# Kernel optimization log

Hardware: AMD Instinct MI355X
Metric: run time of the kernel (lower is better)

## Reference

```python
import jax, jax.numpy as jnp
import numpy as np

N_NODES = 100000
N_EDGES = 600000
VOCAB = 5000
NUM_GRAPHS = 2000
NUM_CLASSES = 10


def setup_inputs() -> dict:
    key = jax.random.key(0)
    ks = jax.random.split(key, 12)
    x = jax.random.randint(ks[0], (N_NODES,), 0, VOCAB, dtype=jnp.int32)
    edge_index = jax.random.randint(ks[1], (2, N_EDGES), 0, N_NODES, dtype=jnp.int32)
    batch = jnp.sort(jax.random.randint(ks[2], (N_NODES,), 0, NUM_GRAPHS, dtype=jnp.int32))
    emb = jax.random.normal(ks[3], (VOCAB, 64), dtype=jnp.float32) * 0.1
    W1 = jax.random.normal(ks[4], (64, 128), dtype=jnp.float32) * (1.0 / np.sqrt(64))
    b1 = jnp.zeros((128,), dtype=jnp.float32)
    W2 = jax.random.normal(ks[5], (128, 128), dtype=jnp.float32) * (1.0 / np.sqrt(128))
    b2 = jnp.zeros((128,), dtype=jnp.float32)
    Wlin = jax.random.normal(ks[6], (128, NUM_CLASSES), dtype=jnp.float32) * (1.0 / np.sqrt(128))
    blin = jnp.zeros((NUM_CLASSES,), dtype=jnp.float32)
    return {"x": x, "edge_index": edge_index, "batch": batch, "num_graphs": NUM_GRAPHS,
            "emb": emb, "W1": W1, "b1": b1, "W2": W2, "b2": b2, "Wlin": Wlin, "blin": blin}


def reference(x, edge_index, batch, num_graphs, emb, W1, b1, W2, b2, Wlin, blin):
    N = x.shape[0]
    loops = jnp.arange(N, dtype=edge_index.dtype)
    src = jnp.concatenate([edge_index[0], loops])  # message sources (j)
    dst = jnp.concatenate([edge_index[1], loops])  # aggregation targets (i)
    # GCN symmetric normalization with self-loops (PyG gcn_norm, source_to_target)
    deg = jax.ops.segment_sum(jnp.ones_like(dst, dtype=jnp.float32), dst, num_segments=N)
    dinv = jnp.where(deg > 0, jax.lax.rsqrt(deg), 0.0)
    norm = dinv[src] * dinv[dst]  # [E+N]

    def gcn(h, W, b):
        h = h @ W  # linear transform first (GCNConv order)
        msg = h[src] * norm[:, None]  # gather + scale, [E+N, F]
        return jax.ops.segment_sum(msg, dst, num_segments=N) + b

    h = emb[x]  # [N, 64]
    h = jax.nn.relu(gcn(h, W1, b1))
    h = jax.nn.relu(gcn(h, W2, b2))
    g = jax.ops.segment_max(h, batch, num_segments=num_graphs)  # global_max_pool
    return g @ Wlin + blin
```

## Files before the change

### kernel.cpp

```cpp
#include <hip/hip_runtime.h>
#include <hip/hip_bf16.h>
#include <hip/hip_fp16.h>


typedef _Float16 h8 __attribute__((ext_vector_type(8)));
typedef float f32x4 __attribute__((ext_vector_type(4)));

__global__ __launch_bounds__(256) void k_zero(int4* __restrict__ deg, int n4i,
                                              int4* __restrict__ pool, int p4i) {
    int t = blockIdx.x * 256 + threadIdx.x;
    int4 z = make_int4(0, 0, 0, 0);
    if (t < n4i) deg[t] = z;
    if (t < p4i) pool[t] = z;
}

__global__ __launch_bounds__(256) void k_degprep(const int* __restrict__ dst, int* __restrict__ deg, int E,
                                                 const float* __restrict__ emb, __half2* __restrict__ e16,
                                                 const float* __restrict__ W1, _Float16* __restrict__ W1T,
                                                 const float* __restrict__ W2, _Float16* __restrict__ W2T,
                                                 int nEmbF, int gE, int nCast) {
    int bid = blockIdx.x;
    if (bid < gE) {
        int e = bid * 256 + threadIdx.x;
        if (e < E) atomicAdd(&deg[dst[e]], 1);
    } else if (bid < gE + nCast) {
        int t = (bid - gE) * 256 + threadIdx.x;
        if (t * 4 < nEmbF) {
            float4 v = *(const float4*)&emb[t * 4];
            e16[t * 2] = __floats2half2_rn(v.x, v.y);
            e16[t * 2 + 1] = __floats2half2_rn(v.z, v.w);
        }
    } else if (bid < gE + nCast + 32) {
        int t = (bid - gE - nCast) * 256 + threadIdx.x;
        int c = t >> 6, k = t & 63;
        W1T[c * 64 + k] = (_Float16)W1[k * 128 + c];
    } else {
        int t = (bid - gE - nCast - 32) * 256 + threadIdx.x;
        if (t < 128 * 128) {
            int c = t >> 7, k = t & 127;
            W2T[c * 128 + k] = (_Float16)W2[k * 128 + c];
        }
    }
}

__global__ __launch_bounds__(256) void k_scan1(const int* __restrict__ deg, int* __restrict__ exc,
                                               int* __restrict__ bsums, float* __restrict__ dinv, int N) {
    __shared__ int s[256];
    int i = blockIdx.x * 256 + threadIdx.x;
    int v = (i < N) ? deg[i] : 0;
    if (i < N) dinv[i] = rsqrtf((float)(v + 1));
    s[threadIdx.x] = v;
    __syncthreads();
    for (int off = 1; off < 256; off <<= 1) {
        int t = (threadIdx.x >= (unsigned)off) ? s[threadIdx.x - off] : 0;
        __syncthreads();
        s[threadIdx.x] += t;
        __syncthreads();
    }
    if (i < N) exc[i] = s[threadIdx.x] - v;
    if (threadIdx.x == 255) bsums[blockIdx.x] = s[255];
}

__global__ __launch_bounds__(512) void k_scan2(int* __restrict__ bsums, int nb) {
    __shared__ int s[512];
    int i = threadIdx.x;
    int v = (i < nb) ? bsums[i] : 0;
    s[i] = v;
    __syncthreads();
    for (int off = 1; off < 512; off <<= 1) {
        int t = (i >= off) ? s[i - off] : 0;
        __syncthreads();
        s[i] += t;
        __syncthreads();
    }
    if (i < nb) bsums[i] = s[i] - v;
}

__global__ __launch_bounds__(256) void k_scan3(int* __restrict__ rowstart, int* __restrict__ cursor,
                                               const int* __restrict__ bsums, int N, int E) {
    int i = blockIdx.x * 256 + threadIdx.x;
    if (i < N) {
        int r = rowstart[i] + bsums[blockIdx.x];
        rowstart[i] = r;
        cursor[i] = r;
    }
    if (i == 0 && blockIdx.x == 0) rowstart[N] = E;
}

__global__ __launch_bounds__(256) void k_fill(const int* __restrict__ src, const int* __restrict__ dst,
                                              const int* __restrict__ x, const float* __restrict__ dinv,
                                              int* __restrict__ cursor, int2* __restrict__ ed,
                                              int* __restrict__ cols, int E) {
    int e = blockIdx.x * 256 + threadIdx.x;
    if (e < E) {
        int d = dst[e];
        int s = src[e];
        int pos = atomicAdd(&cursor[d], 1);
        ed[pos] = make_int2(x[s], __float_as_int(dinv[s]));
        cols[pos] = s;
    }
}

__global__ __launch_bounds__(512) void k_mlp(const __half2* __restrict__ e16, const int* __restrict__ x,
                                             const float* __restrict__ dinv, const int* __restrict__ rs,
                                             const int2* __restrict__ ed, const _Float16* __restrict__ W1T,
                                             const float* __restrict__ b1, const _Float16* __restrict__ W2T,
                                             _Float16* __restrict__ P, int N) {
    __shared__ _Float16 Xs[32][72];
    __shared__ _Float16 Hs[32][136];
    int tid = threadIdx.x;
    int blk0 = blockIdx.x * 32;
    {
        int lane = tid & 31;
        int hw = tid >> 5;
        int p = lane >> 3;
        int f16 = lane & 7;
        const h8* e8 = (const h8*)e16;
        int nlA = hw * 2, nlB = nlA + 1;
        int gA = blk0 + nlA; if (gA >= N) gA = N - 1;
        int gB = blk0 + nlB; if (gB >= N) gB = N - 1;
        int cA0 = rs[gA], cA1 = rs[gA + 1];
        int cB0 = rs[gB], cB1 = rs[gB + 1];
        int baseA = (cA0 < cA1) ? cA1 - 1 : 0;
        int baseB = (cB0 < cB1) ? cB1 - 1 : 0;
        float dA = dinv[gA], dB = dinv[gB];
        h8 selfA = e8[(size_t)x[gA] * 8 + f16];
        h8 selfB = e8[(size_t)x[gB] * 8 + f16];
        float accA[8] = {}, accB[8] = {};
        {
            int eA0 = cA0 + p, eA1 = cA0 + 4 + p;
            int eB0 = cB0 + p, eB1 = cB0 + 4 + p;
            int2 rA0 = ed[(eA0 < cA1) ? eA0 : baseA];
            int2 rA1 = ed[(eA1 < cA1) ? eA1 : baseA];
            int2 rB0 = ed[(eB0 < cB1) ? eB0 : baseB];
            int2 rB1 = ed[(eB1 < cB1) ? eB1 : baseB];
            h8 tA0 = e8[(size_t)rA0.x * 8 + f16];
            h8 tA1 = e8[(size_t)rA1.x * 8 + f16];
            h8 tB0 = e8[(size_t)rB0.x * 8 + f16];
            h8 tB1 = e8[(size_t)rB1.x * 8 + f16];
            float wA0 = (eA0 < cA1) ? __int_as_float(rA0.y) : 0.f;
            float wA1 = (eA1 < cA1) ? __int_as_float(rA1.y) : 0.f;
            float wB0 = (eB0 < cB1) ? __int_as_float(rB0.y) : 0.f;
            float wB1 = (eB1 < cB1) ? __int_as_float(rB1.y) : 0.f;
#pragma unroll
            for (int f = 0; f < 8; ++f) {
                accA[f] = fmaf(wA1, (float)tA1[f], fmaf(wA0, (float)tA0[f], accA[f]));
                accB[f] = fmaf(wB1, (float)tB1[f], fmaf(wB0, (float)tB0[f], accB[f]));
            }
        }
        for (int eb = cA0 + 8; eb < cA1; eb += 8) {
            int e0 = eb + p, e1i = eb + 4 + p;
            int2 r0 = ed[(e0 < cA1) ? e0 : cA1 - 1];
            int2 r1 = ed[(e1i < cA1) ? e1i : cA1 - 1];
            h8 t0 = e8[(size_t)r0.x * 8 + f16];
            h8 t1 = e8[(size_t)r1.x * 8 + f16];
            float w0 = (e0 < cA1) ? __int_as_float(r0.y) : 0.f;
            float w1 = (e1i < cA1) ? __int_as_float(r1.y) : 0.f;
#pragma unroll
            for (int f = 0; f < 8; ++f)
                accA[f] = fmaf(w1, (float)t1[f], fmaf(w0, (float)t0[f], accA[f]));
        }
        for (int eb = cB0 + 8; eb < cB1; eb += 8) {
            int e0 = eb + p, e1i = eb + 4 + p;
            int2 r0 = ed[(e0 < cB1) ? e0 : cB1 - 1];
            int2 r1 = ed[(e1i < cB1) ? e1i : cB1 - 1];
            h8 t0 = e8[(size_t)r0.x * 8 + f16];
            h8 t1 = e8[(size_t)r1.x * 8 + f16];
            float w0 = (e0 < cB1) ? __int_as_float(r0.y) : 0.f;
            float w1 = (e1i < cB1) ? __int_as_float(r1.y) : 0.f;
#pragma unroll
            for (int f = 0; f < 8; ++f)
                accB[f] = fmaf(w1, (float)t1[f], fmaf(w0, (float)t0[f], accB[f]));
        }
        h8 yA, yB;
#pragma unroll
        for (int f = 0; f < 8; ++f) {
            float a = accA[f];
            a += __shfl_xor(a, 8);
            a += __shfl_xor(a, 16);
            float b = accB[f];
            b += __shfl_xor(b, 8);
            b += __shfl_xor(b, 16);
            yA[f] = (_Float16)(dA * fmaf(dA, (float)selfA[f], a));
            yB[f] = (_Float16)(dB * fmaf(dB, (float)selfB[f], b));
        }
        if (p == 0) {
            *(h8*)&Xs[nlA][f16 * 8] = yA;
            *(h8*)&Xs[nlB][f16 * 8] = yB;
        }
    }
    __syncthreads();
    int l = tid & 63, wid = tid >> 6;
    int r = l & 15, kg = l >> 4;
    int rb = wid & 1;
    int ch = wid >> 1;
    {
        f32x4 acc[2];
#pragma unroll
        for (int ct = 0; ct < 2; ++ct) acc[ct] = (f32x4){0.f, 0.f, 0.f, 0.f};
#pragma unroll
        for (int kc = 0; kc < 2; ++kc) {
            h8 a = *(const h8*)&Xs[rb * 16 + r][kc * 32 + kg * 8];
#pragma unroll
            for (int ct = 0; ct < 2; ++ct) {
                h8 b = *(const h8*)(W1T + (size_t)(ch * 32 + ct * 16 + r) * 64 + kc * 32 + kg * 8);
                acc[ct] = __builtin_amdgcn_mfma_f32_16x16x32_f16(a, b, acc[ct], 0, 0, 0);
            }
        }
#pragma unroll
        for (int ct = 0; ct < 2; ++ct) {
            float bias = b1[ch * 32 + ct * 16 + r];
#pragma unroll
            for (int i = 0; i < 4; ++i)
                Hs[rb * 16 + 4 * kg + i][ch * 32 + ct * 16 + r] =
                    (_Float16)fmaxf(acc[ct][i] + bias, 0.f);
        }
    }
    __syncthreads();
    {
        f32x4 acc[2];
#pragma unroll
        for (int ct = 0; ct < 2; ++ct) acc[ct] = (f32x4){0.f, 0.f, 0.f, 0.f};
#pragma unroll
        for (int kc = 0; kc < 4; ++kc) {
            h8 a = *(const h8*)&Hs[rb * 16 + r][kc * 32 + kg * 8];
#pragma unroll
            for (int ct = 0; ct < 2; ++ct) {
                h8 b = *(const h8*)(W2T + (size_t)(ch * 32 + ct * 16 + r) * 128 + kc * 32 + kg * 8);
                acc[ct] = __builtin_amdgcn_mfma_f32_16x16x32_f16(a, b, acc[ct], 0, 0, 0);
            }
        }
        float dv[4];
#pragma unroll
        for (int i = 0; i < 4; ++i) {
            int gr = blk0 + rb * 16 + 4 * kg + i;
            dv[i] = (gr < N) ? dinv[gr] : 0.f;
        }
#pragma unroll
        for (int ct = 0; ct < 2; ++ct) {
#pragma unroll
            for (int i = 0; i < 4; ++i) {
                int gr = blk0 + rb * 16 + 4 * kg + i;
                if (gr < N)
                    P[(size_t)gr * 128 + ch * 32 + ct * 16 + r] = (_Float16)(acc[ct][i] * dv[i]);
            }
        }
    }
}

__global__ __launch_bounds__(256) void k_agg2pool(const h8* __restrict__ P8, const int* __restrict__ batch,
                                                  const float* __restrict__ dinv, const int* __restrict__ rs,
                                                  const int* __restrict__ cols, const float* __restrict__ b2,
                                                  float* __restrict__ pool, int N, int G) {
    __shared__ int lpool[4][128];
    int tid = threadIdx.x;
    lpool[tid >> 7][tid & 127] = 0;
    lpool[(tid >> 7) + 2][tid & 127] = 0;
    __syncthreads();
    int lane = tid & 31;
    int p = lane >> 4;
    int s = lane & 15;
    int blk_n0 = blockIdx.x * 16;
    int gfirst = batch[(blk_n0 < N) ? blk_n0 : (N - 1)];
    int n0 = blk_n0 + (tid >> 5) * 2;
    if (n0 < N) {
        int nA = n0;
        int nB = (n0 + 1 < N) ? n0 + 1 : n0;
        int cA0 = rs[nA], cA1 = rs[nA + 1];
        int cB0 = rs[nB], cB1 = rs[nB + 1];
        bool hasA = cA0 < cA1, hasB = cB0 < cB1;
        h8 sA = P8[(size_t)nA * 16 + s];
        h8 sB = P8[(size_t)nB * 16 + s];
        float aA[8] = {}, aB[8] = {};
        {
            h8 tA[8], tB[8];
            float wA[8], wB[8];
#pragma unroll
            for (int i = 0; i < 8; ++i) {
                int ei = cA0 + 2 * i + p;
                int ec = (ei < cA1) ? ei : (hasA ? cA1 - 1 : 0);
                tA[i] = P8[(size_t)cols[ec] * 16 + s];
                wA[i] = (ei < cA1) ? 1.f : 0.f;
            }
#pragma unroll
            for (int i = 0; i < 8; ++i) {
                int ei = cB0 + 2 * i + p;
                int ec = (ei < cB1) ? ei : (hasB ? cB1 - 1 : 0);
                tB[i] = P8[(size_t)cols[ec] * 16 + s];
                wB[i] = (ei < cB1) ? 1.f : 0.f;
            }
#pragma unroll
            for (int i = 0; i < 8; ++i)
#pragma unroll
                for (int f = 0; f < 8; ++f) aA[f] = fmaf(wA[i], (float)tA[i][f], aA[f]);
#pragma unroll
            for (int i = 0; i < 8; ++i)
#pragma unroll
                for (int f = 0; f < 8; ++f) aB[f] = fmaf(wB[i], (float)tB[i][f], aB[f]);
        }
        for (int eb = cA0 + 16; eb < cA1; eb += 16) {
            h8 t[8];
            float w[8];
#pragma unroll
            for (int i = 0; i < 8; ++i) {
                int ei = eb + 2 * i + p;
                int ec = (ei < cA1) ? ei : cA1 - 1;
                t[i] = P8[(size_t)cols[ec] * 16 + s];
                w[i] = (ei < cA1) ? 1.f : 0.f;
            }
#pragma unroll
            for (int i = 0; i < 8; ++i)
#pragma unroll
                for (int f = 0; f < 8; ++f) aA[f] = fmaf(w[i], (float)t[i][f], aA[f]);
        }
        for (int eb = cB0 + 16; eb < cB1; eb += 16) {
            h8 t[8];
            float w[8];
#pragma unroll
            for (int i = 0; i < 8; ++i) {
                int ei = eb + 2 * i + p;
                int ec = (ei < cB1) ? ei : cB1 - 1;
                t[i] = P8[(size_t)cols[ec] * 16 + s];
                w[i] = (ei < cB1) ? 1.f : 0.f;
            }
#pragma unroll
            for (int i = 0; i < 8; ++i)
#pragma unroll
                for (int f = 0; f < 8; ++f) aB[f] = fmaf(w[i], (float)t[i][f], aB[f]);
        }
        float dA = dinv[nA], dB = dinv[nB];
        int gA = batch[nA], gB = batch[nB];
        float4 bb0 = *(const float4*)&b2[s * 8];
        float4 bb1 = *(const float4*)&b2[s * 8 + 4];
        float bv[8] = {bb0.x, bb0.y, bb0.z, bb0.w, bb1.x, bb1.y, bb1.z, bb1.w};
        float zA[8], zB[8];
#pragma unroll
        for (int f = 0; f < 8; ++f) {
            float a = aA[f] + __shfl_xor(aA[f], 16);
            float b = aB[f] + __shfl_xor(aB[f], 16);
            zA[f] = fmaxf(fmaf(dA, (float)sA[f] + a, bv[f]), 0.f);
            zB[f] = fmaxf(fmaf(dB, (float)sB[f] + b, bv[f]), 0.f);
        }
        auto emit = [&](int g, const float* m) {
            if (p != 0) return;
            int slot = g - gfirst;
            if (slot < 4) {
#pragma unroll
                for (int f = 0; f < 8; ++f) {
                    int ff = (f + s) & 7;
                    if (m[ff] > 0.f) atomicMax(&lpool[slot][s * 8 + ff], __float_as_int(m[ff]));
                }
            } else {
                float* pg = pool + (size_t)g * 128 + s * 8;
#pragma unroll
                for (int f = 0; f < 8; ++f)
                    if (m[f] > 0.f) atomicMax((int*)(pg + f), __float_as_int(m[f]));
            }
        };
        if (gA == gB) {
            float m[8];
#pragma unroll
            for (int f = 0; f < 8; ++f) m[f] = fmaxf(zA[f], zB[f]);
            emit(gA, m);
        } else {
            emit(gA, zA);
            emit(gB, zB);
        }
    }
    __syncthreads();
    {
        int f = tid & 127;
        for (int sl = tid >> 7; sl < 4; sl += 2) {
            int v = lpool[sl][f];
            if (v > 0) atomicMax((int*)&pool[(size_t)(gfirst + sl) * 128 + f], v);
        }
    }
}

__global__ __launch_bounds__(256) void k_final(const float* __restrict__ pool, const float* __restrict__ Wlin,
                                               const float* __restrict__ blin, float* __restrict__ out, int G) {
    int t = blockIdx.x * 256 + threadIdx.x;
    if (t >= G * 10) return;
    int g = t / 10, c = t % 10;
    float acc = blin[c];
    const float* pr = pool + (size_t)g * 128;
#pragma unroll 8
    for (int f = 0; f < 128; ++f) acc = fmaf(pr[f], Wlin[f * 10 + c], acc);
    out[t] = acc;
}

extern "C" void kernel_launch(void* const* d_in, const int* in_sizes, int n_in,
                              void* d_out, int out_size, void* d_ws, size_t ws_size,
                              hipStream_t stream) {
    const int* x = (const int*)d_in[0];
    const int* ei = (const int*)d_in[1];
    const int* batch = (const int*)d_in[2];
    const float* emb = (const float*)d_in[4];
    const float* W1 = (const float*)d_in[5];
    const float* b1 = (const float*)d_in[6];
    const float* W2 = (const float*)d_in[7];
    const float* b2 = (const float*)d_in[8];
    const float* Wlin = (const float*)d_in[9];
    const float* blin = (const float*)d_in[10];
    float* out = (float*)d_out;

    int N = in_sizes[0];
    int E = in_sizes[1] / 2;
    int VOCAB = in_sizes[4] / 64;
    int G = out_size / 10;
    const int* srcp = ei;
    const int* dstp = ei + E;

    char* p = (char*)d_ws;
    auto alloc = [&](size_t bytes) -> char* {
        char* r = p;
        p += (bytes + 255) & ~(size_t)255;
        return r;
    };
    int* deg = (int*)alloc((size_t)N * 4);
    int* cursor = (int*)alloc((size_t)N * 4);
    int* rowstart = (int*)alloc((size_t)(N + 1) * 4);
    int* bsums = (int*)alloc(512 * 4);
    float* dinv = (float*)alloc((size_t)N * 4);
    int2* ed = (int2*)alloc((size_t)E * 8);
    int* cols = (int*)alloc((size_t)E * 4);
    _Float16* e16 = (_Float16*)alloc((size_t)VOCAB * 64 * 2);
    _Float16* W1T = (_Float16*)alloc(128 * 64 * 2);
    _Float16* W2T = (_Float16*)alloc(128 * 128 * 2);
    _Float16* P = (_Float16*)alloc((size_t)N * 128 * 2);
    float* pool = (float*)alloc((size_t)G * 128 * 4);

    int gE = (E + 255) / 256;
    int gN = (N + 255) / 256;
    int nEmbF = VOCAB * 64;
    int nCast = (nEmbF / 4 + 255) / 256;

    int n4i = N / 4, p4i = G * 128 / 4;
    int zg = ((n4i > p4i ? n4i : p4i) + 255) / 256;
    k_zero<<<zg, 256, 0, stream>>>((int4*)deg, n4i, (int4*)pool, p4i);
    k_degprep<<<gE + nCast + 32 + 64, 256, 0, stream>>>(dstp, deg, E, emb, (__half2*)e16, W1, W1T,
                                                        W2, W2T, nEmbF, gE, nCast);
    k_scan1<<<gN, 256, 0, stream>>>(deg, rowstart, bsums, dinv, N);
    k_scan2<<<1, 512, 0, stream>>>(bsums, gN);
    k_scan3<<<gN, 256, 0, stream>>>(rowstart, cursor, bsums, N, E);
    k_fill<<<gE, 256, 0, stream>>>(srcp, dstp, x, dinv, cursor, ed, cols, E);
    k_mlp<<<(N + 31) / 32, 512, 0, stream>>>((const __half2*)e16, x, dinv, rowstart, ed, W1T, b1,
                                             W2T, P, N);
    k_agg2pool<<<(N + 15) / 16, 256, 0, stream>>>((const h8*)P, batch, dinv, rowstart, cols,
                                                  b2, pool, N, G);
    k_final<<<(G * 10 + 255) / 256, 256, 0, stream>>>(pool, Wlin, blin, out, G);
}
```

Measured before the change: 180.3 us.

## Store CSR row ranges as int2 pairs and shrink MLP blocks to 16 nodes

The scan now writes a packed (start,end) int2 per node, so the aggregation kernels fetch each row range with one 8-byte load instead of two dependent 4-byte loads. The MLP kernel is reduced from 32-node, 512-thread blocks to 16-node, 256-thread blocks, each wave computing one 32-column slice of one 16-row tile. This is meant to raise block count and occupancy and cut LDS use per block. In exchange, the weight tiles are reloaded by twice as many blocks, and the scan needs an extra workspace array.

```diff
diff --git a/kernel.cpp b/kernel.cpp
--- a/kernel.cpp
+++ b/kernel.cpp
@@ -76,15 +76,16 @@
     if (i < nb) bsums[i] = s[i] - v;
 }
 
-__global__ __launch_bounds__(256) void k_scan3(int* __restrict__ rowstart, int* __restrict__ cursor,
-                                               const int* __restrict__ bsums, int N, int E) {
+__global__ __launch_bounds__(256) void k_scan3(const int* __restrict__ exc, int* __restrict__ cursor,
+                                               const int* __restrict__ bsums, int2* __restrict__ rse,
+                                               int N, int E) {
     int i = blockIdx.x * 256 + threadIdx.x;
     if (i < N) {
-        int r = rowstart[i] + bsums[blockIdx.x];
-        rowstart[i] = r;
+        int r = exc[i] + bsums[blockIdx.x];
+        int rn = (i + 1 < N) ? exc[i + 1] + bsums[(i + 1) >> 8] : E;
         cursor[i] = r;
-    }
-    if (i == 0 && blockIdx.x == 0) rowstart[N] = E;
+        rse[i] = make_int2(r, rn);
+    }
 }
 
 __global__ __launch_bounds__(256) void k_fill(const int* __restrict__ src, const int* __restrict__ dst,
@@ -101,15 +102,15 @@
     }
 }
 
-__global__ __launch_bounds__(512) void k_mlp(const __half2* __restrict__ e16, const int* __restrict__ x,
-                                             const float* __restrict__ dinv, const int* __restrict__ rs,
+__global__ __launch_bounds__(256) void k_mlp(const __half2* __restrict__ e16, const int* __restrict__ x,
+                                             const float* __restrict__ dinv, const int2* __restrict__ rse,
                                              const int2* __restrict__ ed, const _Float16* __restrict__ W1T,
                                              const float* __restrict__ b1, const _Float16* __restrict__ W2T,
                                              _Float16* __restrict__ P, int N) {
-    __shared__ _Float16 Xs[32][72];
-    __shared__ _Float16 Hs[32][136];
+    __shared__ _Float16 Xs[16][72];
+    __shared__ _Float16 Hs[16][136];
     int tid = threadIdx.x;
-    int blk0 = blockIdx.x * 32;
+    int blk0 = blockIdx.x * 16;
     {
         int lane = tid & 31;
         int hw = tid >> 5;
@@ -119,8 +120,10 @@
         int nlA = hw * 2, nlB = nlA + 1;
         int gA = blk0 + nlA; if (gA >= N) gA = N - 1;
         int gB = blk0 + nlB; if (gB >= N) gB = N - 1;
-        int cA0 = rs[gA], cA1 = rs[gA + 1];
-        int cB0 = rs[gB], cB1 = rs[gB + 1];
+        int2 rA = rse[gA];
+        int2 rB = rse[gB];
+        int cA0 = rA.x, cA1 = rA.y;
+        int cB0 = rB.x, cB1 = rB.y;
         int baseA = (cA0 < cA1) ? cA1 - 1 : 0;
         int baseB = (cB0 < cB1) ? cB1 - 1 : 0;
         float dA = dinv[gA], dB = dinv[gB];
@@ -192,15 +195,14 @@
     __syncthreads();
     int l = tid & 63, wid = tid >> 6;
     int r = l & 15, kg = l >> 4;
-    int rb = wid & 1;
-    int ch = wid >> 1;
+    int ch = wid;
     {
         f32x4 acc[2];
 #pragma unroll
         for (int ct = 0; ct < 2; ++ct) acc[ct] = (f32x4){0.f, 0.f, 0.f, 0.f};
 #pragma unroll
         for (int kc = 0; kc < 2; ++kc) {
-            h8 a = *(const h8*)&Xs[rb * 16 + r][kc * 32 + kg * 8];
+            h8 a = *(const h8*)&Xs[r][kc * 32 + kg * 8];
 #pragma unroll
             for (int ct = 0; ct < 2; ++ct) {
                 h8 b = *(const h8*)(W1T + (size_t)(ch * 32 + ct * 16 + r) * 64 + kc * 32 + kg * 8);
@@ -212,8 +214,7 @@
             float bias = b1[ch * 32 + ct * 16 + r];
 #pragma unroll
             for (int i = 0; i < 4; ++i)
-                Hs[rb * 16 + 4 * kg + i][ch * 32 + ct * 16 + r] =
-                    (_Float16)fmaxf(acc[ct][i] + bias, 0.f);
+                Hs[4 * kg + i][ch * 32 + ct * 16 + r] = (_Float16)fmaxf(acc[ct][i] + bias, 0.f);
         }
     }
     __syncthreads();
@@ -223,7 +224,7 @@
         for (int ct = 0; ct < 2; ++ct) acc[ct] = (f32x4){0.f, 0.f, 0.f, 0.f};
 #pragma unroll
         for (int kc = 0; kc < 4; ++kc) {
-            h8 a = *(const h8*)&Hs[rb * 16 + r][kc * 32 + kg * 8];
+            h8 a = *(const h8*)&Hs[r][kc * 32 + kg * 8];
 #pragma unroll
             for (int ct = 0; ct < 2; ++ct) {
                 h8 b = *(const h8*)(W2T + (size_t)(ch * 32 + ct * 16 + r) * 128 + kc * 32 + kg * 8);
@@ -233,14 +234,14 @@
         float dv[4];
 #pragma unroll
         for (int i = 0; i < 4; ++i) {
-            int gr = blk0 + rb * 16 + 4 * kg + i;
+            int gr = blk0 + 4 * kg + i;
             dv[i] = (gr < N) ? dinv[gr] : 0.f;
         }
 #pragma unroll
         for (int ct = 0; ct < 2; ++ct) {
 #pragma unroll
             for (int i = 0; i < 4; ++i) {
-                int gr = blk0 + rb * 16 + 4 * kg + i;
+                int gr = blk0 + 4 * kg + i;
                 if (gr < N)
                     P[(size_t)gr * 128 + ch * 32 + ct * 16 + r] = (_Float16)(acc[ct][i] * dv[i]);
             }
@@ -249,7 +250,7 @@
 }
 
 __global__ __launch_bounds__(256) void k_agg2pool(const h8* __restrict__ P8, const int* __restrict__ batch,
-                                                  const float* __restrict__ dinv, const int* __restrict__ rs,
+                                                  const float* __restrict__ dinv, const int2* __restrict__ rse,
                                                   const int* __restrict__ cols, const float* __restrict__ b2,
                                                   float* __restrict__ pool, int N, int G) {
     __shared__ int lpool[4][128];
@@ -266,8 +267,10 @@
     if (n0 < N) {
         int nA = n0;
         int nB = (n0 + 1 < N) ? n0 + 1 : n0;
-        int cA0 = rs[nA], cA1 = rs[nA + 1];
-        int cB0 = rs[nB], cB1 = rs[nB + 1];
+        int2 rA = rse[nA];
+        int2 rB = rse[nB];
+        int cA0 = rA.x, cA1 = rA.y;
+        int cB0 = rB.x, cB1 = rB.y;
         bool hasA = cA0 < cA1, hasB = cB0 < cB1;
         h8 sA = P8[(size_t)nA * 16 + s];
         h8 sB = P8[(size_t)nB * 16 + s];
@@ -418,8 +421,9 @@
         return r;
     };
     int* deg = (int*)alloc((size_t)N * 4);
+    int* exc = (int*)alloc((size_t)N * 4);
     int* cursor = (int*)alloc((size_t)N * 4);
-    int* rowstart = (int*)alloc((size_t)(N + 1) * 4);
+    int2* rse = (int2*)alloc((size_t)N * 8);
     int* bsums = (int*)alloc(512 * 4);
     float* dinv = (float*)alloc((size_t)N * 4);
     int2* ed = (int2*)alloc((size_t)E * 8);
@@ -440,13 +444,13 @@
     k_zero<<<zg, 256, 0, stream>>>((int4*)deg, n4i, (int4*)pool, p4i);
     k_degprep<<<gE + nCast + 32 + 64, 256, 0, stream>>>(dstp, deg, E, emb, (__half2*)e16, W1, W1T,
                                                         W2, W2T, nEmbF, gE, nCast);
-    k_scan1<<<gN, 256, 0, stream>>>(deg, rowstart, bsums, dinv, N);
+    k_scan1<<<gN, 256, 0, stream>>>(deg, exc, bsums, dinv, N);
     k_scan2<<<1, 512, 0, stream>>>(bsums, gN);
-    k_scan3<<<gN, 256, 0, stream>>>(rowstart, cursor, bsums, N, E);
+    k_scan3<<<gN, 256, 0, stream>>>(exc, cursor, bsums, rse, N, E);
     k_fill<<<gE, 256, 0, stream>>>(srcp, dstp, x, dinv, cursor, ed, cols, E);
-    k_mlp<<<(N + 31) / 32, 512, 0, stream>>>((const __half2*)e16, x, dinv, rowstart, ed, W1T, b1,
+    k_mlp<<<(N + 15) / 16, 256, 0, stream>>>((const __half2*)e16, x, dinv, rse, ed, W1T, b1,
                                              W2T, P, N);
-    k_agg2pool<<<(N + 15) / 16, 256, 0, stream>>>((const h8*)P, batch, dinv, rowstart, cols,
+    k_agg2pool<<<(N + 15) / 16, 256, 0, stream>>>((const h8*)P, batch, dinv, rse, cols,
                                                   b2, pool, N, G);
     k_final<<<(G * 10 + 255) / 256, 256, 0, stream>>>(pool, Wlin, blin, out, G);
 }
```

After: 182.7 us. About the same (+1.3%).
